# Optimization experiments

Hardware: AMD Instinct MI355X
Metric: run time of the kernel (lower is better)

## Reference

```python
import jax, jax.numpy as jnp
import numpy as np
from jax import lax

H_STEP = 1.0 / 3.0  # h = (t1 - t0) / N with t0=0, t1=1, N=3
N_STEPS = 3


def _conv(x, w):
    # x: [B, C, H, W], w: [O, I, kh, kw], 'same' padding, stride 1
    return lax.conv_general_dilated(
        x, w, window_strides=(1, 1), padding='SAME',
        dimension_numbers=('NCHW', 'OIHW', 'NCHW'))


def setup_inputs() -> dict:
    key = jax.random.key(0)
    ks = jax.random.split(key, 5)
    B, C, H, W = 16, 128, 128, 128
    fan_in = C * 9
    return {
        'x': jax.random.normal(ks[0], (B, C, H, W), dtype=jnp.float32),
        'w1': jax.random.normal(ks[1], (C, C, 3, 3), dtype=jnp.float32) * (2.0 / fan_in) ** 0.5,
        'b1': jax.random.normal(ks[2], (C,), dtype=jnp.float32) * 0.01,
        'w2': jax.random.normal(ks[3], (C, C, 3, 3), dtype=jnp.float32) * (2.0 / fan_in) ** 0.5,
        'b2': jax.random.normal(ks[4], (C,), dtype=jnp.float32) * 0.01,
    }


def reference(x, w1, b1, w2, b2):
    # Euler-step residual block: x <- x + h * conv2(relu(conv1(x))) for N steps
    for _ in range(N_STEPS):
        t = jax.nn.relu(_conv(x, w1) + b1[None, :, None, None])
        x = x + H_STEP * (_conv(t, w2) + b2[None, :, None, None])
    return jax.nn.relu(x)
```

## Files before the change

### kernel.cpp

```cpp
#include <hip/hip_runtime.h>
#include <hip/hip_bf16.h>


#define BATCH 16
#define CH    128
#define HH    128
#define WW    128
#define H_STEP (1.0f/3.0f)

#define CI_PAD 136

typedef short bf16x8 __attribute__((ext_vector_type(8)));
typedef float f32x4  __attribute__((ext_vector_type(4)));

__device__ __forceinline__ float bf2f(unsigned short u) {
    union { unsigned int i; float f; } c; c.i = ((unsigned int)u) << 16; return c.f;
}
__device__ __forceinline__ unsigned short f2bf(float f) {
    union { float f; unsigned int i; } c; c.f = f;
    unsigned int i = c.i;
    return (unsigned short)((i + 0x7FFFu + ((i >> 16) & 1u)) >> 16);
}

__global__ __launch_bounds__(256)
void transpose_x(const float* __restrict__ x, unsigned short* __restrict__ xb)
{
    __shared__ unsigned short s[128 * 132];
    const int tid = threadIdx.x;
    const int bz  = blockIdx.x;
    const int b = bz >> 7, y = bz & 127;

    #pragma unroll
    for (int it = 0; it < 16; ++it) {
        int idx = it * 256 + tid;
        int ci = idx >> 5, xq = idx & 31;
        float4 v = *(const float4*)&x[(((size_t)b * CH + ci) * HH + y) * WW + xq * 4];
        uint2 p;
        p.x = (unsigned int)f2bf(v.x) | ((unsigned int)f2bf(v.y) << 16);
        p.y = (unsigned int)f2bf(v.z) | ((unsigned int)f2bf(v.w) << 16);
        *(uint2*)&s[ci * 132 + xq * 4] = p;
    }
    __syncthreads();
    #pragma unroll
    for (int it = 0; it < 8; ++it) {
        int idx = it * 256 + tid;
        int xx = idx >> 4, cc = idx & 15;
        unsigned short t[8];
        #pragma unroll
        for (int k = 0; k < 8; ++k) t[k] = s[(cc * 8 + k) * 132 + xx];
        uint4 p;
        p.x = (unsigned int)t[0] | ((unsigned int)t[1] << 16);
        p.y = (unsigned int)t[2] | ((unsigned int)t[3] << 16);
        p.z = (unsigned int)t[4] | ((unsigned int)t[5] << 16);
        p.w = (unsigned int)t[6] | ((unsigned int)t[7] << 16);
        *(uint4*)&xb[((size_t)(b * HH + y) * WW + xx) * CH + cc * 8] = p;
    }
}

__global__ __launch_bounds__(256)
void convert_w(const float* __restrict__ w, unsigned short* __restrict__ wb)
{
    int idx = blockIdx.x * 256 + threadIdx.x;
    #pragma unroll
    for (int t = 0; t < 9; ++t)
        wb[t * 16384 + idx] = f2bf(w[(size_t)idx * 9 + t]);
}

template<int MODE>
__global__ __launch_bounds__(256, 2)
void conv_mfma(const unsigned short* __restrict__ in,
               const unsigned short* __restrict__ wb,
               const float* __restrict__ bias,
               const unsigned short* resb,
               unsigned short* outb,
               float* __restrict__ outf)
{
    __shared__ unsigned short s_in[130 * CI_PAD];
    __shared__ unsigned short s_w [128 * CI_PAD];

    const int tid = threadIdx.x;
    const int bz  = blockIdx.x;
    const int b = bz >> 7, y = bz & 127;

    const int lane = tid & 63;
    const int wid  = tid >> 6;
    const int woc0 = (wid >> 1) * 64;
    const int wpx0 = (wid & 1) * 64;
    const int n16  = lane & 15;
    const int q    = lane >> 4;

    f32x4 acc[4][4];
    #pragma unroll
    for (int i = 0; i < 4; ++i)
        #pragma unroll
        for (int j = 0; j < 4; ++j) acc[i][j] = (f32x4)0.0f;

    if (tid < 34) {
        int r  = (tid < 17) ? 0 : 129;
        int cc = (tid < 17) ? tid : tid - 17;
        uint4 z = {0u, 0u, 0u, 0u};
        *(uint4*)&s_in[r * CI_PAD + cc * 8] = z;
    }

    for (int ky = 0; ky < 3; ++ky) {
        const int gy = y + ky - 1;
        if (gy < 0 || gy >= HH) continue;
        const size_t inrow = ((size_t)(b * HH + gy) * WW) * CH;

        for (int kx = 0; kx < 3; ++kx) {
            __syncthreads();
            if (kx == 0) {
                #pragma unroll
                for (int it = 0; it < 8; ++it) {
                    int idx = it * 256 + tid;
                    int x = idx >> 4, cc = idx & 15;
                    uint4 v = *(const uint4*)&in[inrow + (size_t)x * CH + cc * 8];
                    *(uint4*)&s_in[(x + 1) * CI_PAD + cc * 8] = v;
                }
            }
            const unsigned short* wt = wb + (ky * 3 + kx) * 16384;
            #pragma unroll
            for (int it = 0; it < 8; ++it) {
                int idx = it * 256 + tid;
                int oc = idx >> 4, cc = idx & 15;
                uint4 v = *(const uint4*)&wt[oc * 128 + cc * 8];
                *(uint4*)&s_w[oc * CI_PAD + cc * 8] = v;
            }
            __syncthreads();

            #pragma unroll
            for (int c0 = 0; c0 < 128; c0 += 32) {
                bf16x8 af[4], bfr[4];
                #pragma unroll
                for (int i = 0; i < 4; ++i)
                    af[i] = *(const bf16x8*)&s_w[(woc0 + i * 16 + n16) * CI_PAD + c0 + q * 8];
                #pragma unroll
                for (int j = 0; j < 4; ++j)
                    bfr[j] = *(const bf16x8*)&s_in[(wpx0 + j * 16 + n16 + kx) * CI_PAD + c0 + q * 8];
                #pragma unroll
                for (int i = 0; i < 4; ++i)
                    #pragma unroll
                    for (int j = 0; j < 4; ++j)
                        acc[i][j] = __builtin_amdgcn_mfma_f32_16x16x32_bf16(
                            af[i], bfr[j], acc[i][j], 0, 0, 0);
            }
        }
    }

    const int ybase = (b * HH + y) * WW;
    if (MODE == 0 || MODE == 1) {
        #pragma unroll
        for (int j = 0; j < 4; ++j) {
            int x = wpx0 + j * 16 + n16;
            size_t pbase = (size_t)(ybase + x) * CH;
            #pragma unroll
            for (int i = 0; i < 4; ++i) {
                int oc0 = woc0 + i * 16 + q * 4;
                float v0 = acc[i][j][0] + bias[oc0 + 0];
                float v1 = acc[i][j][1] + bias[oc0 + 1];
                float v2 = acc[i][j][2] + bias[oc0 + 2];
                float v3 = acc[i][j][3] + bias[oc0 + 3];
                if (MODE == 0) {
                    v0 = fmaxf(v0, 0.f); v1 = fmaxf(v1, 0.f);
                    v2 = fmaxf(v2, 0.f); v3 = fmaxf(v3, 0.f);
                } else {
                    uint2 rr = *(const uint2*)&resb[pbase + oc0];
                    v0 = bf2f((unsigned short)(rr.x & 0xffff)) + H_STEP * v0;
                    v1 = bf2f((unsigned short)(rr.x >> 16))    + H_STEP * v1;
                    v2 = bf2f((unsigned short)(rr.y & 0xffff)) + H_STEP * v2;
                    v3 = bf2f((unsigned short)(rr.y >> 16))    + H_STEP * v3;
                }
                uint2 po;
                po.x = (unsigned int)f2bf(v0) | ((unsigned int)f2bf(v1) << 16);
                po.y = (unsigned int)f2bf(v2) | ((unsigned int)f2bf(v3) << 16);
                *(uint2*)&outb[pbase + oc0] = po;
            }
        }
    } else {
        #pragma unroll
        for (int i = 0; i < 4; ++i) {
            #pragma unroll
            for (int r = 0; r < 4; ++r) {
                int oc = woc0 + i * 16 + q * 4 + r;
                float bv = bias[oc];
                size_t orow = ((size_t)(b * CH + oc) * HH + y) * WW;
                #pragma unroll
                for (int j = 0; j < 4; ++j) {
                    int x = wpx0 + j * 16 + n16;
                    float v = acc[i][j][r] + bv;
                    v = bf2f(resb[(size_t)(ybase + x) * CH + oc]) + H_STEP * v;
                    outf[orow + x] = fmaxf(v, 0.f);
                }
            }
        }
    }
}

extern "C" void kernel_launch(void* const* d_in, const int* in_sizes, int n_in,
                              void* d_out, int out_size, void* d_ws, size_t ws_size,
                              hipStream_t stream) {
    const float* x0 = (const float*)d_in[0];
    const float* w1 = (const float*)d_in[1];
    const float* b1 = (const float*)d_in[2];
    const float* w2 = (const float*)d_in[3];
    const float* b2 = (const float*)d_in[4];

    const size_t NELEM = (size_t)BATCH * CH * HH * WW;
    unsigned short* XB = (unsigned short*)d_ws;
    unsigned short* T  = XB + NELEM;

    unsigned short* WB1;
    if (ws_size >= NELEM * 4 + 2 * 294912)
        WB1 = T + NELEM;
    else
        WB1 = (unsigned short*)d_in[0];
    unsigned short* WB2 = WB1 + 9 * 16384;

    dim3 block(256);
    dim3 gridRow(BATCH * HH);

    transpose_x<<<gridRow, block, 0, stream>>>(x0, XB);
    convert_w<<<dim3(64), block, 0, stream>>>(w1, WB1);
    convert_w<<<dim3(64), block, 0, stream>>>(w2, WB2);

    conv_mfma<0><<<gridRow, block, 0, stream>>>(XB, WB1, b1, nullptr, T, nullptr);
    conv_mfma<1><<<gridRow, block, 0, stream>>>(T, WB2, b2, XB, XB, nullptr);
    conv_mfma<0><<<gridRow, block, 0, stream>>>(XB, WB1, b1, nullptr, T, nullptr);
    conv_mfma<1><<<gridRow, block, 0, stream>>>(T, WB2, b2, XB, XB, nullptr);
    conv_mfma<0><<<gridRow, block, 0, stream>>>(XB, WB1, b1, nullptr, T, nullptr);
    conv_mfma<2><<<gridRow, block, 0, stream>>>(T, WB2, b2, XB, nullptr, (float*)d_out);
}
```

Baseline: 800.2 us.

## Stream conv operands via async global-to-LDS loads with XOR swizzle and double-buffered weights

Replaces the register-staged global-to-shared copies with direct global_load_lds transfers. The padded shared layouts become XOR-swizzled unpadded ones so that bank conflicts stay low. Weight tiles are split into 64-channel halves and double-buffered, so the next tap's weights load while the current half is computed. Border rows are skipped through precomputed ky bounds, and block indices are remapped to improve cache locality. The cost is an extra barrier per stage and swizzle address arithmetic, and the input row reload still stalls at each ky boundary.

```diff
diff --git a/kernel.cpp b/kernel.cpp
--- a/kernel.cpp
+++ b/kernel.cpp
@@ -8,8 +8,6 @@
 #define WW    128
 #define H_STEP (1.0f/3.0f)
 
-#define CI_PAD 136
-
 typedef short bf16x8 __attribute__((ext_vector_type(8)));
 typedef float f32x4  __attribute__((ext_vector_type(4)));
 
@@ -20,6 +18,12 @@
     union { float f; unsigned int i; } c; c.f = f;
     unsigned int i = c.i;
     return (unsigned short)((i + 0x7FFFu + ((i >> 16) & 1u)) >> 16);
+}
+
+__device__ __forceinline__ void gload16(const unsigned short* g, unsigned short* l) {
+    __builtin_amdgcn_global_load_lds(
+        (const __attribute__((address_space(1))) unsigned int*)g,
+        (__attribute__((address_space(3))) unsigned int*)l, 16, 0, 0);
 }
 
 __global__ __launch_bounds__(256)
@@ -75,11 +79,12 @@
                unsigned short* outb,
                float* __restrict__ outf)
 {
-    __shared__ unsigned short s_in[130 * CI_PAD];
-    __shared__ unsigned short s_w [128 * CI_PAD];
+    __shared__ unsigned short s_in[130 * CH];
+    __shared__ unsigned short s_w [2][128 * 64];
 
     const int tid = threadIdx.x;
-    const int bz  = blockIdx.x;
+    const int bz0 = blockIdx.x;
+    const int bz  = ((bz0 & 7) << 8) | (bz0 >> 3);
     const int b = bz >> 7, y = bz & 127;
 
     const int lane = tid & 63;
@@ -89,61 +94,98 @@
     const int n16  = lane & 15;
     const int q    = lane >> 4;
 
+    const int wr   = lane >> 3;
+    const int wc   = lane & 7;
+    const int w_lane_elem = wr * CH + ((wc ^ wr) << 3);
+    const int xl   = lane >> 4;
+    const int ch16 = lane & 15;
+
+    const int kylo = (y == 0)      ? 1 : 0;
+    const int kyhi = (y == HH - 1) ? 1 : 2;
+    const int NS   = (kyhi - kylo + 1) * 6;
+
     f32x4 acc[4][4];
     #pragma unroll
     for (int i = 0; i < 4; ++i)
         #pragma unroll
         for (int j = 0; j < 4; ++j) acc[i][j] = (f32x4)0.0f;
 
-    if (tid < 34) {
-        int r  = (tid < 17) ? 0 : 129;
-        int cc = (tid < 17) ? tid : tid - 17;
+    if (tid < 32) {
+        int r  = (tid < 16) ? 0 : 129;
+        int cc = tid & 15;
         uint4 z = {0u, 0u, 0u, 0u};
-        *(uint4*)&s_in[r * CI_PAD + cc * 8] = z;
-    }
-
-    for (int ky = 0; ky < 3; ++ky) {
-        const int gy = y + ky - 1;
-        if (gy < 0 || gy >= HH) continue;
+        *(uint4*)&s_in[r * CH + cc * 8] = z;
+    }
+
+    auto stage_in = [&](int gy) {
         const size_t inrow = ((size_t)(b * HH + gy) * WW) * CH;
-
-        for (int kx = 0; kx < 3; ++kx) {
-            __syncthreads();
-            if (kx == 0) {
-                #pragma unroll
-                for (int it = 0; it < 8; ++it) {
-                    int idx = it * 256 + tid;
-                    int x = idx >> 4, cc = idx & 15;
-                    uint4 v = *(const uint4*)&in[inrow + (size_t)x * CH + cc * 8];
-                    *(uint4*)&s_in[(x + 1) * CI_PAD + cc * 8] = v;
-                }
-            }
-            const unsigned short* wt = wb + (ky * 3 + kx) * 16384;
-            #pragma unroll
-            for (int it = 0; it < 8; ++it) {
-                int idx = it * 256 + tid;
-                int oc = idx >> 4, cc = idx & 15;
-                uint4 v = *(const uint4*)&wt[oc * 128 + cc * 8];
-                *(uint4*)&s_w[oc * CI_PAD + cc * 8] = v;
-            }
-            __syncthreads();
-
-            #pragma unroll
-            for (int c0 = 0; c0 < 128; c0 += 32) {
-                bf16x8 af[4], bfr[4];
-                #pragma unroll
-                for (int i = 0; i < 4; ++i)
-                    af[i] = *(const bf16x8*)&s_w[(woc0 + i * 16 + n16) * CI_PAD + c0 + q * 8];
+        #pragma unroll
+        for (int c = 0; c < 8; ++c) {
+            int x   = wid * 32 + c * 4 + xl;
+            int swz = (x + 1) & 7;
+            const unsigned short* src = in + inrow + (size_t)x * CH + ((ch16 ^ swz) << 3);
+            unsigned short* dst = (unsigned short*)s_in + CH + (wid * 8 + c) * 512;
+            gload16(src, dst);
+        }
+    };
+    auto stage_w = [&](int tap, int kh, int buf) {
+        const unsigned short* wt = wb + tap * 16384 + kh * 64;
+        #pragma unroll
+        for (int c = 0; c < 4; ++c) {
+            int base_r = (wid * 4 + c) * 8;
+            const unsigned short* src = wt + base_r * CH + w_lane_elem;
+            unsigned short* dst = &s_w[buf][(wid * 4 + c) * 512];
+            gload16(src, dst);
+        }
+    };
+
+    stage_in(y + kylo - 1);
+    stage_w(kylo * 3, 0, 0);
+    __syncthreads();
+
+    for (int s = 0; s < NS; ++s) {
+        const int cur = s & 1;
+        const int kyi = s / 6;
+        const int r6  = s - kyi * 6;
+        const int kx  = r6 >> 1;
+        const int kh  = s & 1;
+
+        if (s + 1 < NS) {
+            const int s1  = s + 1;
+            const int ky1 = s1 / 6;
+            const int r61 = s1 - ky1 * 6;
+            stage_w((kylo + ky1) * 3 + (r61 >> 1), s1 & 1, cur ^ 1);
+        }
+
+        #pragma unroll
+        for (int c0 = 0; c0 < 64; c0 += 32) {
+            bf16x8 af[4], bfr[4];
+            const int cqa = (c0 >> 3) + q;
+            #pragma unroll
+            for (int i = 0; i < 4; ++i) {
+                int row = woc0 + i * 16 + n16;
+                af[i] = *(const bf16x8*)&s_w[cur][row * 64 + ((cqa ^ (row & 7)) << 3)];
+            }
+            const int cqb = kh * 8 + (c0 >> 3) + q;
+            #pragma unroll
+            for (int j = 0; j < 4; ++j) {
+                int rowb = wpx0 + j * 16 + n16 + kx;
+                bfr[j] = *(const bf16x8*)&s_in[rowb * CH + ((cqb ^ (rowb & 7)) << 3)];
+            }
+            #pragma unroll
+            for (int i = 0; i < 4; ++i)
                 #pragma unroll
                 for (int j = 0; j < 4; ++j)
-                    bfr[j] = *(const bf16x8*)&s_in[(wpx0 + j * 16 + n16 + kx) * CI_PAD + c0 + q * 8];
-                #pragma unroll
-                for (int i = 0; i < 4; ++i)
-                    #pragma unroll
-                    for (int j = 0; j < 4; ++j)
-                        acc[i][j] = __builtin_amdgcn_mfma_f32_16x16x32_bf16(
-                            af[i], bfr[j], acc[i][j], 0, 0, 0);
-            }
+                    acc[i][j] = __builtin_amdgcn_mfma_f32_16x16x32_bf16(
+                        af[i], bfr[j], acc[i][j], 0, 0, 0);
+        }
+
+        if (r6 == 5 && s + 1 < NS) {
+            __syncthreads();
+            stage_in(y + (kylo + kyi + 1) - 1);
+            __syncthreads();
+        } else {
+            __syncthreads();
         }
     }
 
```

Result: no change. 800.0 us (-0.0%).
